# Performance work log

Hardware: AMD Instinct MI355X
Metric: run time of the kernel (lower is better)

The kernel has to match this reference:

```python
import jax, jax.numpy as jnp
import numpy as np

EMBED, HEADS, LEVELS, POINTS = 256, 8, 4, 4
HD = EMBED // HEADS
BS, NQ = 2, 16384
SHAPES = [(128, 128), (64, 64), (32, 32), (16, 16)]  # (H, W) per level
NV = sum(h * w for h, w in SHAPES)
EPS = 1e-5


def layernorm(x, g, b):
    mu = jnp.mean(x, -1, keepdims=True)
    var = jnp.mean((x - mu) ** 2, -1, keepdims=True)
    return (x - mu) / jnp.sqrt(var + EPS) * g + b


def bilinear_sample(vl, loc, H, W):
    # vl: (bs, heads, H*W, hd); loc: (bs, nq, heads, P, 2) normalized [0,1]
    # grid_sample semantics: align_corners=False, zero padding
    x = loc[..., 0] * W - 0.5
    y = loc[..., 1] * H - 0.5
    x0 = jnp.floor(x)
    y0 = jnp.floor(y)
    lx, ly = x - x0, y - y0
    x0 = x0.astype(jnp.int32)
    y0 = y0.astype(jnp.int32)
    gather = jax.vmap(jax.vmap(lambda t, i: t[i]))  # over (bs, heads)
    acc = None
    for dx, dy, w in ((0, 0, (1 - lx) * (1 - ly)), (1, 0, lx * (1 - ly)),
                      (0, 1, (1 - lx) * ly), (1, 1, lx * ly)):
        xi, yi = x0 + dx, y0 + dy
        valid = ((xi >= 0) & (xi < W) & (yi >= 0) & (yi < H)).astype(vl.dtype)
        idx = jnp.clip(yi, 0, H - 1) * W + jnp.clip(xi, 0, W - 1)
        idx = idx.transpose(0, 2, 1, 3)           # (bs, heads, nq, P)
        g = gather(vl, idx)                       # (bs, heads, nq, P, hd)
        wv = (w * valid).transpose(0, 2, 1, 3)[..., None]
        acc = g * wv if acc is None else acc + g * wv
    return acc


def forward(lidar_feat, feat_flatten, ref_2d, spatial_shapes, level_start_index,
            q_pose, W_off, b_off, W_attn, b_attn, W_val, b_val, W_out, b_out,
            ln1_g, ln1_b, ffn_w1, ffn_w2, ln2_g, ln2_b):
    identity = lidar_feat                         # (nq, bs, C)
    q = (lidar_feat + q_pose).transpose(1, 0, 2)  # (bs, nq, C)
    bs, nq, C = q.shape
    v = feat_flatten.transpose(1, 0, 2) @ W_val + b_val
    v = v.reshape(bs, -1, HEADS, HD)
    off = (q @ W_off + b_off).reshape(bs, nq, HEADS, LEVELS, POINTS, 2)
    aw = (q @ W_attn + b_attn).reshape(bs, nq, HEADS, LEVELS * POINTS)
    aw = jax.nn.softmax(aw, -1).reshape(bs, nq, HEADS, LEVELS, POINTS)
    ss = np.asarray(spatial_shapes)               # static level shapes
    lsi = np.asarray(level_start_index)
    norm = jnp.asarray(ss[:, ::-1].copy(), q.dtype)  # (L, 2) [W, H]
    loc = ref_2d[:, :, None, :, None, :] + off / norm[None, None, None, :, None, :]
    out = jnp.zeros((bs, nq, HEADS, HD), q.dtype)
    for l in range(LEVELS):
        H, W = int(ss[l, 0]), int(ss[l, 1])
        s = int(lsi[l])
        vl = v[:, s:s + H * W].transpose(0, 2, 1, 3)   # (bs, heads, HW, hd)
        sampled = bilinear_sample(vl, loc[:, :, :, l], H, W)
        out = out + jnp.einsum('bhqpd,bqhp->bqhd', sampled, aw[:, :, :, l, :])
    out = out.reshape(bs, nq, C) @ W_out + b_out
    out = out.transpose(1, 0, 2) + identity       # residual (dropout=eval noop)
    x = layernorm(out, ln1_g, ln1_b)
    x = layernorm(jnp.maximum(x @ ffn_w1, 0.0) @ ffn_w2 + x, ln2_g, ln2_b)
    return x


def setup_inputs():
    key = jax.random.key(0)
    ks = jax.random.split(key, 16)
    starts = np.cumsum([0] + [h * w for h, w in SHAPES])[:-1]
    d = {
        'lidar_feat': jax.random.normal(ks[0], (NQ, BS, EMBED), jnp.float32),
        'feat_flatten': jax.random.normal(ks[1], (NV, BS, EMBED), jnp.float32),
        'ref_2d': jax.random.uniform(ks[2], (BS, NQ, LEVELS, 2), jnp.float32),
        'spatial_shapes': jnp.array(SHAPES, jnp.int32),
        'level_start_index': jnp.array(starts, jnp.int32),
        'q_pose': jax.random.normal(ks[3], (NQ, BS, EMBED), jnp.float32),
        'W_off': 0.02 * jax.random.normal(ks[4], (EMBED, HEADS * LEVELS * POINTS * 2), jnp.float32),
        'b_off': 2.0 * jax.random.normal(ks[5], (HEADS * LEVELS * POINTS * 2,), jnp.float32),
        'W_attn': 0.02 * jax.random.normal(ks[6], (EMBED, HEADS * LEVELS * POINTS), jnp.float32),
        'b_attn': jnp.zeros((HEADS * LEVELS * POINTS,), jnp.float32),
        'W_val': 0.02 * jax.random.normal(ks[7], (EMBED, EMBED), jnp.float32),
        'b_val': jnp.zeros((EMBED,), jnp.float32),
        'W_out': 0.02 * jax.random.normal(ks[8], (EMBED, EMBED), jnp.float32),
        'b_out': jnp.zeros((EMBED,), jnp.float32),
        'ln1_g': jnp.ones((EMBED,), jnp.float32),
        'ln1_b': jnp.zeros((EMBED,), jnp.float32),
        'ffn_w1': 0.02 * jax.random.normal(ks[9], (EMBED, EMBED), jnp.float32),
        'ffn_w2': 0.02 * jax.random.normal(ks[10], (EMBED, EMBED), jnp.float32),
        'ln2_g': jnp.ones((EMBED,), jnp.float32),
        'ln2_b': jnp.zeros((EMBED,), jnp.float32),
    }
    return d


def reference(lidar_feat, feat_flatten, ref_2d, spatial_shapes, level_start_index,
              q_pose, W_off, b_off, W_attn, b_attn, W_val, b_val, W_out, b_out,
              ln1_g, ln1_b, ffn_w1, ffn_w2, ln2_g, ln2_b):
    return forward(lidar_feat, feat_flatten, ref_2d, spatial_shapes,
                   level_start_index, q_pose, W_off, b_off, W_attn, b_attn,
                   W_val, b_val, W_out, b_out, ln1_g, ln1_b, ffn_w1, ffn_w2,
                   ln2_g, ln2_b)
```

## Files before the change

kernel.cpp:

```cpp
#include <hip/hip_runtime.h>
#include <cstdint>

#define EMBED 256
#define HEADS 8
#define LEVELS 4
#define POINTS 4
#define BS 2
#define NQ 16384
#define NV 21760
#define MQ (BS*NQ)
#define MV (BS*NV)
#define VAL_BLK 340
#define OA_BLK  256

typedef __attribute__((ext_vector_type(8))) short short8;
typedef __attribute__((ext_vector_type(4))) float f32x4;

__device__ __forceinline__ unsigned short f2bf(float f) {
    unsigned int u = __float_as_uint(f);
    u = (u + 0x7FFFu + ((u >> 16) & 1u)) >> 16;
    return (unsigned short)u;
}
__device__ __forceinline__ float bf2f(unsigned short h) {
    return __uint_as_float(((unsigned int)h) << 16);
}
__device__ __forceinline__ void glds16(const unsigned short* g, unsigned short* l) {
    __builtin_amdgcn_global_load_lds((const __attribute__((address_space(1))) void*)g,
                                     (__attribute__((address_space(3))) void*)l, 16, 0, 0);
}

struct WtArgs {
    const float* src[6];
    unsigned short* dst[6];
    int n[6];
};
__global__ __launch_bounds__(256) void prep_wt(
    WtArgs a, const float* __restrict__ ref2d,
    int* __restrict__ bkt, int* __restrict__ hist)
{
    const int t = threadIdx.x, g = blockIdx.y, bx = blockIdx.x;
    if (g == 6) {
        if (bx < 64) {
#pragma unroll
            for (int i = 0; i < 2; ++i) {
                const int rb = bx * 512 + i * 256 + t;
                const float x = ref2d[(size_t)rb * 8 + 0];
                const float y = ref2d[(size_t)rb * 8 + 1];
                const int qx = min(15, max(0, (int)(x * 16.f)));
                const int qy = min(15, max(0, (int)(y * 16.f)));
                const int bv = (rb >> 14) * 256 + qy * 16 + qx;
                bkt[rb] = bv;
                atomicAdd(&hist[bv], 1);
            }
        }
        return;
    }
    const int N = a.n[g];
    const int e = bx * 256 + t;
    if (e >= 256 * N) return;
    const int k = e / N, n = e - k * N;
    a.dst[g][(size_t)n * 256 + k] = f2bf(a.src[g][e]);
}

template<int NCOLS>
__device__ __forceinline__ void gemm_core(
    unsigned short* As, unsigned short* Bs, int bx,
    const float* __restrict__ Af, const float* __restrict__ A2f, int inner,
    const unsigned short* __restrict__ Bt,
    const float* __restrict__ bias0, const float* __restrict__ bias1,
    float* __restrict__ outf, unsigned short* __restrict__ outh)
{
    constexpr int FN = NCOLS / 64;
    const int t = threadIdx.x, l = t & 63, w = t >> 6;
    const int wm = w >> 2, wn = w & 3;
    const int frow = l & 15, fgrp = l >> 4;
    const size_t brow = (size_t)bx * 128;

    const int fslot = fgrp ^ ((frow & 3) ^ ((frow >> 2) & 3));
    const int srow = l >> 2;
    const int sswz = (l & 3) ^ ((srow & 3) ^ ((srow >> 2) & 3));
    const unsigned short* gB0 = Bt + ((size_t)(w * 16 + srow)) * 256 + sswz * 8;

    const int arow_s = t >> 2, aslot_s = t & 3;
    const int grow = (int)brow + arow_s;
    const int bidx = grow / inner, nn = grow - bidx * inner;
    const float* srcA = Af + (size_t)(nn * BS + bidx) * 256;
    const float* srcA2 = A2f ? A2f + (size_t)(nn * BS + bidx) * 256 : nullptr;
    const int aswz_s = aslot_s ^ ((arow_s & 3) ^ ((arow_s >> 2) & 3));

    f32x4 acc[4][FN];
#pragma unroll
    for (int i = 0; i < 4; ++i)
#pragma unroll
        for (int j = 0; j < FN; ++j) acc[i][j] = f32x4{0.f, 0.f, 0.f, 0.f};

    float4 pA0 = *(const float4*)(srcA + aslot_s * 8);
    float4 pA1 = *(const float4*)(srcA + aslot_s * 8 + 4);
    float4 pC0, pC1;
    if (srcA2) { pC0 = *(const float4*)(srcA2 + aslot_s * 8);
                 pC1 = *(const float4*)(srcA2 + aslot_s * 8 + 4); }

    for (int k0 = 0; k0 < 256; k0 += 32) {
        glds16(gB0 + k0,         &Bs[w * 512]);
        glds16(gB0 + 32768 + k0, &Bs[(w + 8) * 512]);
        if constexpr (NCOLS == 384)
            glds16(gB0 + 65536 + k0, &Bs[(w + 16) * 512]);

        float c[8] = {pA0.x, pA0.y, pA0.z, pA0.w, pA1.x, pA1.y, pA1.z, pA1.w};
        if (srcA2) {
            c[0] += pC0.x; c[1] += pC0.y; c[2] += pC0.z; c[3] += pC0.w;
            c[4] += pC1.x; c[5] += pC1.y; c[6] += pC1.z; c[7] += pC1.w;
        }
        short8 pk;
#pragma unroll
        for (int i = 0; i < 8; ++i) pk[i] = (short)f2bf(c[i]);
        *reinterpret_cast<short8*>(&As[arow_s * 32 + aswz_s * 8]) = pk;
        if (k0 + 32 < 256) {
            pA0 = *(const float4*)(srcA + k0 + 32 + aslot_s * 8);
            pA1 = *(const float4*)(srcA + k0 + 32 + aslot_s * 8 + 4);
            if (srcA2) { pC0 = *(const float4*)(srcA2 + k0 + 32 + aslot_s * 8);
                         pC1 = *(const float4*)(srcA2 + k0 + 32 + aslot_s * 8 + 4); }
        }
        __syncthreads();

        short8 af[4]; short8 bq[FN];
#pragma unroll
        for (int fm = 0; fm < 4; ++fm)
            af[fm] = *reinterpret_cast<const short8*>(&As[(wm * 64 + fm * 16 + frow) * 32 + fslot * 8]);
#pragma unroll
        for (int fn = 0; fn < FN; ++fn)
            bq[fn] = *reinterpret_cast<const short8*>(&Bs[(wn * (NCOLS / 4) + fn * 16 + frow) * 32 + fslot * 8]);
#pragma unroll
        for (int fm = 0; fm < 4; ++fm)
#pragma unroll
            for (int fn = 0; fn < FN; ++fn)
                acc[fm][fn] = __builtin_amdgcn_mfma_f32_16x16x32_bf16(af[fm], bq[fn], acc[fm][fn], 0, 0, 0);
        __syncthreads();
    }

#pragma unroll
    for (int fn = 0; fn < FN; ++fn) {
        const int col = wn * (NCOLS / 4) + fn * 16 + frow;
        float b = 0.f;
        if (NCOLS == 384) b = (col < 256) ? bias0[col] : bias1[col - 256];
        else              b = bias0[col];
#pragma unroll
        for (int fm = 0; fm < 4; ++fm)
#pragma unroll
            for (int j = 0; j < 4; ++j) {
                const size_t row = brow + wm * 64 + fm * 16 + fgrp * 4 + j;
                const float x = acc[fm][fn][j] + b;
                if (outf) outf[row * NCOLS + col] = x;
                else      outh[row * NCOLS + col] = f2bf(x);
            }
    }
}

__global__ __launch_bounds__(512) void valoa_k(
    const float* __restrict__ feat, const float* __restrict__ lidar,
    const float* __restrict__ q_pose,
    const unsigned short* __restrict__ wt_val, const unsigned short* __restrict__ wt_oa,
    const float* __restrict__ b_val, const float* __restrict__ b_off,
    const float* __restrict__ b_attn,
    float* __restrict__ vb, unsigned short* __restrict__ oa,
    const int* __restrict__ hist, const int* __restrict__ bkt,
    int* __restrict__ perm)
{
    __shared__ unsigned short As[128 * 32];
    __shared__ unsigned short Bs[384 * 32];
    const int bx = blockIdx.x;
    if (bx < VAL_BLK) {
        gemm_core<256>(As, Bs, bx, feat, nullptr, NV, wt_val, b_val, nullptr, vb, nullptr);
    } else if (bx < VAL_BLK + OA_BLK) {
        gemm_core<384>(As, Bs, bx - VAL_BLK, lidar, q_pose, NQ, wt_oa, b_off, b_attn, nullptr, oa);
    } else {
        int* s   = (int*)As;
        int* cur = ((int*)As) + 512;
        const int t = threadIdx.x;
        const int v = hist[t];
        s[t] = v;
        __syncthreads();
        int acc = v;
#pragma unroll
        for (int o = 1; o < 512; o <<= 1) {
            const int add = (t >= o) ? s[t - o] : 0;
            __syncthreads();
            acc += add;
            s[t] = acc;
            __syncthreads();
        }
        cur[t] = acc - v;
        __syncthreads();
#pragma unroll 4
        for (int i = 0; i < 64; ++i) {
            const int rb = i * 512 + t;
            const int pos = atomicAdd(&cur[bkt[rb]], 1);
            perm[pos] = rb;
        }
    }
}

__global__ __launch_bounds__(256) void sampler_k(
    const unsigned short* __restrict__ oa,
    const float* __restrict__ ref2d,
    const float* __restrict__ v,
    const int* __restrict__ perm,
    unsigned short* __restrict__ outh)
{
    const int bid = blockIdx.x;
    const int sbid = (bid & 7) * (MQ / 4 / 8) + (bid >> 3);
    const int q0 = sbid * 4;
    const int t = threadIdx.x;

    __shared__ uint2 s_d[4][8][4][17];

#pragma unroll
    for (int it = 0; it < 2; ++it) {
        const int item = t + it * 256;
        const int tq = item >> 7, hlp = item & 127;
        const int h = hlp >> 4, lp = hlp & 15, li = lp >> 2;
        const int rb = perm[q0 + tq];
        const int b = rb >> 14;

        const float2 refv = *(const float2*)(ref2d + (size_t)rb * 8 + li * 2);
        const ushort2 offu = *(const ushort2*)(oa + (size_t)rb * 384 + hlp * 2);
        const float ax = bf2f(oa[(size_t)rb * 384 + 256 + hlp]);

        float m = ax;
#pragma unroll
        for (int o = 1; o < 16; o <<= 1) m = fmaxf(m, __shfl_xor(m, o));
        const float e = __expf(ax - m);
        float sden = e;
#pragma unroll
        for (int o = 1; o < 16; o <<= 1) sden += __shfl_xor(sden, o);
        const float a = e / sden;

        const int Wl[4]  = {128, 64, 32, 16};
        const int S0l[4] = {0, 16384, 20480, 21504};
        const int Wi = Wl[li]; const float Wf = (float)Wi;
        const float x = (refv.x + bf2f(offu.x) / Wf) * Wf - 0.5f;
        const float y = (refv.y + bf2f(offu.y) / Wf) * Wf - 0.5f;
        const float x0f = floorf(x), y0f = floorf(y);
        const float lx = x - x0f, ly = y - y0f;
        const int x0 = (int)x0f, y0 = (int)y0f;
        const float cw[4] = {(1.f - lx) * (1.f - ly) * a, lx * (1.f - ly) * a,
                             (1.f - lx) * ly * a,          lx * ly * a};
        const int base = b * NV + S0l[li];
#pragma unroll
        for (int c = 0; c < 4; ++c) {
            const int xi = x0 + (c & 1), yi = y0 + (c >> 1);
            const bool val = (xi >= 0) & (xi < Wi) & (yi >= 0) & (yi < Wi);
            const int xc = min(max(xi, 0), Wi - 1), yc = min(max(yi, 0), Wi - 1);
            const unsigned int ofs = (unsigned int)(base + yc * Wi + xc) * 1024u + h * 128u;
            s_d[tq][h][c][lp] = make_uint2(__float_as_uint(val ? cw[c] : 0.f), ofs);
        }
    }
    __syncthreads();

    const int tq = t >> 6, l = t & 63, h = l >> 3, dq = l & 7;
    const int rb = perm[q0 + tq], b = rb >> 14, qi = rb & (NQ - 1);
    const char* vq = (const char*)v + dq * 16u;
    float a0 = 0.f, a1 = 0.f, a2 = 0.f, a3 = 0.f;
#pragma unroll
    for (int c = 0; c < 4; ++c) {
#pragma unroll
        for (int i = 0; i < 16; ++i) {
            const uint2 dd = s_d[tq][h][c][i];
            const float4 raw = *(const float4*)(vq + dd.y);
            const float wgt = __uint_as_float(dd.x);
            a0 += wgt * raw.x;
            a1 += wgt * raw.y;
            a2 += wgt * raw.z;
            a3 += wgt * raw.w;
        }
    }
    ushort4 o; o.x = f2bf(a0); o.y = f2bf(a1); o.z = f2bf(a2); o.w = f2bf(a3);
    *(ushort4*)(outh + (size_t)(qi * BS + b) * 256 + h * 32 + dq * 4) = o;
}

__global__ __launch_bounds__(512) void mega_k(
    const unsigned short* __restrict__ smp, const float* __restrict__ lidar,
    const unsigned short* __restrict__ Wo, const unsigned short* __restrict__ W1,
    const unsigned short* __restrict__ W2, const float* __restrict__ b_out,
    const float* __restrict__ ln1g, const float* __restrict__ ln1b,
    const float* __restrict__ ln2g, const float* __restrict__ ln2b,
    float* __restrict__ outf)
{
    __shared__ unsigned short XH[64 * 256];
    __shared__ unsigned short Bs[256 * 32];
    __shared__ float2 sdLN[64][4];

    const int t = threadIdx.x, l = t & 63, w = t >> 6;
    const int wm = w >> 2, wn = w & 3;
    const int frow = l & 15, fgrp = l >> 4;
    const size_t brow = (size_t)blockIdx.x * 64;

    const int fslot = fgrp ^ ((frow & 3) ^ ((frow >> 2) & 3));
    const int srow = l >> 2;
    const int sswz = (l & 3) ^ ((srow & 3) ^ ((srow >> 2) & 3));

    const unsigned short* gA  = smp + (brow + (size_t)((w & 3) * 16 + srow)) * 256 + sswz * 8;
    const unsigned short* gWo = Wo + ((size_t)(w * 16 + srow)) * 256 + sswz * 8;
    const unsigned short* gW1 = W1 + ((size_t)(w * 16 + srow)) * 256 + sswz * 8;
    const unsigned short* gW2 = W2 + ((size_t)(w * 16 + srow)) * 256 + sswz * 8;

    f32x4 acc[2][4];
    f32x4 xres[2][4];

#pragma unroll
    for (int i = 0; i < 2; ++i)
#pragma unroll
        for (int j = 0; j < 4; ++j) acc[i][j] = f32x4{0.f, 0.f, 0.f, 0.f};

    for (int k0 = 0; k0 < 256; k0 += 32) {
        glds16(gWo + k0,         &Bs[w * 512]);
        glds16(gWo + 32768 + k0, &Bs[(w + 8) * 512]);
        if (w < 4) glds16(gA + k0, &XH[w * 512]);
        __syncthreads();
        short8 af[2], bq[4];
#pragma unroll
        for (int fm = 0; fm < 2; ++fm)
            af[fm] = *reinterpret_cast<const short8*>(&XH[(wm * 32 + fm * 16 + frow) * 32 + fslot * 8]);
#pragma unroll
        for (int fn = 0; fn < 4; ++fn)
            bq[fn] = *reinterpret_cast<const short8*>(&Bs[(wn * 64 + fn * 16 + frow) * 32 + fslot * 8]);
#pragma unroll
        for (int fm = 0; fm < 2; ++fm)
#pragma unroll
            for (int fn = 0; fn < 4; ++fn)
                acc[fm][fn] = __builtin_amdgcn_mfma_f32_16x16x32_bf16(af[fm], bq[fn], acc[fm][fn], 0, 0, 0);
        __syncthreads();
    }

#pragma unroll
    for (int fm = 0; fm < 2; ++fm)
#pragma unroll
        for (int fn = 0; fn < 4; ++fn) {
            const int col = wn * 64 + fn * 16 + frow;
            const float bv = b_out[col];
#pragma unroll
            for (int j = 0; j < 4; ++j) {
                const size_t row = brow + wm * 32 + fm * 16 + fgrp * 4 + j;
                acc[fm][fn][j] += bv + lidar[row * 256 + col];
            }
        }
#pragma unroll
    for (int fm = 0; fm < 2; ++fm)
#pragma unroll
        for (int j = 0; j < 4; ++j) {
            float s1 = 0.f, s2 = 0.f;
#pragma unroll
            for (int fn = 0; fn < 4; ++fn) { const float x = acc[fm][fn][j]; s1 += x; s2 += x * x; }
#pragma unroll
            for (int o = 1; o < 16; o <<= 1) { s1 += __shfl_xor(s1, o); s2 += __shfl_xor(s2, o); }
            if (frow == 0) sdLN[wm * 32 + fm * 16 + fgrp * 4 + j][wn] = make_float2(s1, s2);
        }
    __syncthreads();
#pragma unroll
    for (int fm = 0; fm < 2; ++fm)
#pragma unroll
        for (int j = 0; j < 4; ++j) {
            const int rl = wm * 32 + fm * 16 + fgrp * 4 + j;
            const float2 p0 = sdLN[rl][0], p1 = sdLN[rl][1], p2 = sdLN[rl][2], p3 = sdLN[rl][3];
            const float s1 = p0.x + p1.x + p2.x + p3.x;
            const float s2 = p0.y + p1.y + p2.y + p3.y;
            const float mu = s1 * (1.f / 256.f);
            const float var = s2 * (1.f / 256.f) - mu * mu;
            const float rstd = rsqrtf(var + 1e-5f);
#pragma unroll
            for (int fn = 0; fn < 4; ++fn) {
                const int col = wn * 64 + fn * 16 + frow;
                const float y = (acc[fm][fn][j] - mu) * rstd * ln1g[col] + ln1b[col];
                xres[fm][fn][j] = y;
                const int ss = (col >> 3) ^ (rl & 7);
                XH[rl * 256 + ss * 8 + (col & 7)] = f2bf(y);
            }
        }
    __syncthreads();

#pragma unroll
    for (int i = 0; i < 2; ++i)
#pragma unroll
        for (int j = 0; j < 4; ++j) acc[i][j] = f32x4{0.f, 0.f, 0.f, 0.f};

    for (int k0 = 0; k0 < 256; k0 += 32) {
        glds16(gW1 + k0,         &Bs[w * 512]);
        glds16(gW1 + 32768 + k0, &Bs[(w + 8) * 512]);
        __syncthreads();
        short8 af[2], bq[4];
#pragma unroll
        for (int fm = 0; fm < 2; ++fm) {
            const int row = wm * 32 + fm * 16 + frow;
            const int ss = ((k0 >> 3) + fgrp) ^ (row & 7);
            af[fm] = *reinterpret_cast<const short8*>(&XH[row * 256 + ss * 8]);
        }
#pragma unroll
        for (int fn = 0; fn < 4; ++fn)
            bq[fn] = *reinterpret_cast<const short8*>(&Bs[(wn * 64 + fn * 16 + frow) * 32 + fslot * 8]);
#pragma unroll
        for (int fm = 0; fm < 2; ++fm)
#pragma unroll
            for (int fn = 0; fn < 4; ++fn)
                acc[fm][fn] = __builtin_amdgcn_mfma_f32_16x16x32_bf16(af[fm], bq[fn], acc[fm][fn], 0, 0, 0);
        __syncthreads();
    }

#pragma unroll
    for (int fm = 0; fm < 2; ++fm)
#pragma unroll
        for (int fn = 0; fn < 4; ++fn) {
            const int col = wn * 64 + fn * 16 + frow;
#pragma unroll
            for (int j = 0; j < 4; ++j) {
                const int rl = wm * 32 + fm * 16 + fgrp * 4 + j;
                const int ss = (col >> 3) ^ (rl & 7);
                XH[rl * 256 + ss * 8 + (col & 7)] = f2bf(fmaxf(acc[fm][fn][j], 0.f));
            }
        }
    __syncthreads();

#pragma unroll
    for (int i = 0; i < 2; ++i)
#pragma unroll
        for (int j = 0; j < 4; ++j) acc[i][j] = f32x4{0.f, 0.f, 0.f, 0.f};

    for (int k0 = 0; k0 < 256; k0 += 32) {
        glds16(gW2 + k0,         &Bs[w * 512]);
        glds16(gW2 + 32768 + k0, &Bs[(w + 8) * 512]);
        __syncthreads();
        short8 af[2], bq[4];
#pragma unroll
        for (int fm = 0; fm < 2; ++fm) {
            const int row = wm * 32 + fm * 16 + frow;
            const int ss = ((k0 >> 3) + fgrp) ^ (row & 7);
            af[fm] = *reinterpret_cast<const short8*>(&XH[row * 256 + ss * 8]);
        }
#pragma unroll
        for (int fn = 0; fn < 4; ++fn)
            bq[fn] = *reinterpret_cast<const short8*>(&Bs[(wn * 64 + fn * 16 + frow) * 32 + fslot * 8]);
#pragma unroll
        for (int fm = 0; fm < 2; ++fm)
#pragma unroll
            for (int fn = 0; fn < 4; ++fn)
                acc[fm][fn] = __builtin_amdgcn_mfma_f32_16x16x32_bf16(af[fm], bq[fn], acc[fm][fn], 0, 0, 0);
        __syncthreads();
    }

#pragma unroll
    for (int fm = 0; fm < 2; ++fm)
#pragma unroll
        for (int fn = 0; fn < 4; ++fn)
#pragma unroll
            for (int j = 0; j < 4; ++j) acc[fm][fn][j] += xres[fm][fn][j];
#pragma unroll
    for (int fm = 0; fm < 2; ++fm)
#pragma unroll
        for (int j = 0; j < 4; ++j) {
            float s1 = 0.f, s2 = 0.f;
#pragma unroll
            for (int fn = 0; fn < 4; ++fn) { const float x = acc[fm][fn][j]; s1 += x; s2 += x * x; }
#pragma unroll
            for (int o = 1; o < 16; o <<= 1) { s1 += __shfl_xor(s1, o); s2 += __shfl_xor(s2, o); }
            if (frow == 0) sdLN[wm * 32 + fm * 16 + fgrp * 4 + j][wn] = make_float2(s1, s2);
        }
    __syncthreads();
#pragma unroll
    for (int fm = 0; fm < 2; ++fm)
#pragma unroll
        for (int j = 0; j < 4; ++j) {
            const int rl = wm * 32 + fm * 16 + fgrp * 4 + j;
            const float2 p0 = sdLN[rl][0], p1 = sdLN[rl][1], p2 = sdLN[rl][2], p3 = sdLN[rl][3];
            const float s1 = p0.x + p1.x + p2.x + p3.x;
            const float s2 = p0.y + p1.y + p2.y + p3.y;
            const float mu = s1 * (1.f / 256.f);
            const float var = s2 * (1.f / 256.f) - mu * mu;
            const float rstd = rsqrtf(var + 1e-5f);
            const size_t row = brow + rl;
#pragma unroll
            for (int fn = 0; fn < 4; ++fn) {
                const int col = wn * 64 + fn * 16 + frow;
                outf[row * 256 + col] = (acc[fm][fn][j] - mu) * rstd * ln2g[col] + ln2b[col];
            }
        }
}

extern "C" void kernel_launch(void* const* d_in, const int* in_sizes, int n_in,
                              void* d_out, int out_size, void* d_ws, size_t ws_size,
                              hipStream_t stream)
{
    const float* lidar  = (const float*)d_in[0];
    const float* feat   = (const float*)d_in[1];
    const float* ref2d  = (const float*)d_in[2];
    const float* q_pose = (const float*)d_in[5];
    const float* W_off  = (const float*)d_in[6];
    const float* b_off  = (const float*)d_in[7];
    const float* W_attn = (const float*)d_in[8];
    const float* b_attn = (const float*)d_in[9];
    const float* W_val  = (const float*)d_in[10];
    const float* b_val  = (const float*)d_in[11];
    const float* W_out  = (const float*)d_in[12];
    const float* b_out  = (const float*)d_in[13];
    const float* ln1_g  = (const float*)d_in[14];
    const float* ln1_b  = (const float*)d_in[15];
    const float* ffn_w1 = (const float*)d_in[16];
    const float* ffn_w2 = (const float*)d_in[17];
    const float* ln2_g  = (const float*)d_in[18];
    const float* ln2_b  = (const float*)d_in[19];

    float* out = (float*)d_out;
    char*  ws  = (char*)d_ws;

    float*          vb   = (float*)(ws + 0);
    unsigned short* oa   = (unsigned short*)(ws + 44564480);
    unsigned short* smp  = (unsigned short*)(ws + 69730304);
    unsigned short* wt   = (unsigned short*)(ws + 86507520);
    int* perm = (int*)(ws + 87228416);
    int* bkt  = (int*)(ws + 87359488);
    int* hist = (int*)(ws + 87490560);
    unsigned short* wt_val = wt;
    unsigned short* wt_oa  = wt + 65536;
    unsigned short* wt_out = wt + 163840;
    unsigned short* wt_f1  = wt + 229376;
    unsigned short* wt_f2  = wt + 294912;

    WtArgs wa;
    wa.src[0] = W_val;  wa.dst[0] = wt_val;          wa.n[0] = 256;
    wa.src[1] = W_off;  wa.dst[1] = wt_oa;           wa.n[1] = 256;
    wa.src[2] = W_attn; wa.dst[2] = wt_oa + 65536;   wa.n[2] = 128;
    wa.src[3] = W_out;  wa.dst[3] = wt_out;          wa.n[3] = 256;
    wa.src[4] = ffn_w1; wa.dst[4] = wt_f1;           wa.n[4] = 256;
    wa.src[5] = ffn_w2; wa.dst[5] = wt_f2;           wa.n[5] = 256;

    hipMemsetAsync(hist, 0, 2048, stream);

    prep_wt<<<dim3(384, 7), dim3(256), 0, stream>>>(wa, ref2d, bkt, hist);

    valoa_k<<<dim3(VAL_BLK + OA_BLK + 1), dim3(512), 0, stream>>>(
        feat, lidar, q_pose, wt_val, wt_oa, b_val, b_off, b_attn,
        vb, oa, hist, bkt, perm);

    sampler_k<<<dim3(MQ / 4), dim3(256), 0, stream>>>(oa, ref2d, vb, perm, smp);

    mega_k<<<dim3(MQ / 64), dim3(512), 0, stream>>>(
        smp, lidar, wt_out, wt_f1, wt_f2, b_out,
        ln1_g, ln1_b, ln2_g, ln2_b, out);
}
```

Baseline: 220.4 us.

## Store value projection and lidar residual in bf16 to halve sampler gather traffic

```diff
diff --git a/kernel.cpp b/kernel.cpp
--- a/kernel.cpp
+++ b/kernel.cpp
@@ -23,6 +23,12 @@
 }
 __device__ __forceinline__ float bf2f(unsigned short h) {
     return __uint_as_float(((unsigned int)h) << 16);
+}
+__device__ __forceinline__ float bflo(unsigned int u) {
+    return __uint_as_float(u << 16);
+}
+__device__ __forceinline__ float bfhi(unsigned int u) {
+    return __uint_as_float(u & 0xFFFF0000u);
 }
 __device__ __forceinline__ void glds16(const unsigned short* g, unsigned short* l) {
     __builtin_amdgcn_global_load_lds((const __attribute__((address_space(1))) void*)g,
@@ -68,7 +74,7 @@
     const float* __restrict__ Af, const float* __restrict__ A2f, int inner,
     const unsigned short* __restrict__ Bt,
     const float* __restrict__ bias0, const float* __restrict__ bias1,
-    float* __restrict__ outf, unsigned short* __restrict__ outh)
+    unsigned short* __restrict__ lidarb, unsigned short* __restrict__ outh)
 {
     constexpr int FN = NCOLS / 64;
     const int t = threadIdx.x, l = t & 63, w = t >> 6;
@@ -84,8 +90,9 @@
     const int arow_s = t >> 2, aslot_s = t & 3;
     const int grow = (int)brow + arow_s;
     const int bidx = grow / inner, nn = grow - bidx * inner;
-    const float* srcA = Af + (size_t)(nn * BS + bidx) * 256;
-    const float* srcA2 = A2f ? A2f + (size_t)(nn * BS + bidx) * 256 : nullptr;
+    const size_t srcrow = (size_t)(nn * BS + bidx) * 256;
+    const float* srcA = Af + srcrow;
+    const float* srcA2 = A2f ? A2f + srcrow : nullptr;
     const int aswz_s = aslot_s ^ ((arow_s & 3) ^ ((arow_s >> 2) & 3));
 
     f32x4 acc[4][FN];
@@ -105,6 +112,15 @@
         glds16(gB0 + 32768 + k0, &Bs[(w + 8) * 512]);
         if constexpr (NCOLS == 384)
             glds16(gB0 + 65536 + k0, &Bs[(w + 16) * 512]);
+
+        if (lidarb) {
+            short8 lk;
+            lk[0] = (short)f2bf(pA0.x); lk[1] = (short)f2bf(pA0.y);
+            lk[2] = (short)f2bf(pA0.z); lk[3] = (short)f2bf(pA0.w);
+            lk[4] = (short)f2bf(pA1.x); lk[5] = (short)f2bf(pA1.y);
+            lk[6] = (short)f2bf(pA1.z); lk[7] = (short)f2bf(pA1.w);
+            *reinterpret_cast<short8*>(lidarb + srcrow + k0 + aslot_s * 8) = lk;
+        }
 
         float c[8] = {pA0.x, pA0.y, pA0.z, pA0.w, pA1.x, pA1.y, pA1.z, pA1.w};
         if (srcA2) {
@@ -149,9 +165,7 @@
 #pragma unroll
             for (int j = 0; j < 4; ++j) {
                 const size_t row = brow + wm * 64 + fm * 16 + fgrp * 4 + j;
-                const float x = acc[fm][fn][j] + b;
-                if (outf) outf[row * NCOLS + col] = x;
-                else      outh[row * NCOLS + col] = f2bf(x);
+                outh[row * NCOLS + col] = f2bf(acc[fm][fn][j] + b);
             }
     }
 }
@@ -162,7 +176,8 @@
     const unsigned short* __restrict__ wt_val, const unsigned short* __restrict__ wt_oa,
     const float* __restrict__ b_val, const float* __restrict__ b_off,
     const float* __restrict__ b_attn,
-    float* __restrict__ vb, unsigned short* __restrict__ oa,
+    unsigned short* __restrict__ vb, unsigned short* __restrict__ oa,
+    unsigned short* __restrict__ lidarb,
     const int* __restrict__ hist, const int* __restrict__ bkt,
     int* __restrict__ perm)
 {
@@ -170,9 +185,9 @@
     __shared__ unsigned short Bs[384 * 32];
     const int bx = blockIdx.x;
     if (bx < VAL_BLK) {
-        gemm_core<256>(As, Bs, bx, feat, nullptr, NV, wt_val, b_val, nullptr, vb, nullptr);
+        gemm_core<256>(As, Bs, bx, feat, nullptr, NV, wt_val, b_val, nullptr, nullptr, vb);
     } else if (bx < VAL_BLK + OA_BLK) {
-        gemm_core<384>(As, Bs, bx - VAL_BLK, lidar, q_pose, NQ, wt_oa, b_off, b_attn, nullptr, oa);
+        gemm_core<384>(As, Bs, bx - VAL_BLK, lidar, q_pose, NQ, wt_oa, b_off, b_attn, lidarb, oa);
     } else {
         int* s   = (int*)As;
         int* cur = ((int*)As) + 512;
@@ -200,10 +215,10 @@
     }
 }
 
-__global__ __launch_bounds__(256) void sampler_k(
+__global__ __launch_bounds__(128) void sampler_k(
     const unsigned short* __restrict__ oa,
     const float* __restrict__ ref2d,
-    const float* __restrict__ v,
+    const unsigned short* __restrict__ v,
     const int* __restrict__ perm,
     unsigned short* __restrict__ outh)
 {
@@ -215,8 +230,8 @@
     __shared__ uint2 s_d[4][8][4][17];
 
 #pragma unroll
-    for (int it = 0; it < 2; ++it) {
-        const int item = t + it * 256;
+    for (int it = 0; it < 4; ++it) {
+        const int item = t + it * 128;
         const int tq = item >> 7, hlp = item & 127;
         const int h = hlp >> 4, lp = hlp & 15, li = lp >> 2;
         const int rb = perm[q0 + tq];
@@ -251,35 +266,40 @@
             const int xi = x0 + (c & 1), yi = y0 + (c >> 1);
             const bool val = (xi >= 0) & (xi < Wi) & (yi >= 0) & (yi < Wi);
             const int xc = min(max(xi, 0), Wi - 1), yc = min(max(yi, 0), Wi - 1);
-            const unsigned int ofs = (unsigned int)(base + yc * Wi + xc) * 1024u + h * 128u;
+            const unsigned int ofs = (unsigned int)(base + yc * Wi + xc) * 512u + h * 64u;
             s_d[tq][h][c][lp] = make_uint2(__float_as_uint(val ? cw[c] : 0.f), ofs);
         }
     }
     __syncthreads();
 
-    const int tq = t >> 6, l = t & 63, h = l >> 3, dq = l & 7;
+    const int tq = t >> 5, r = t & 31, h = r >> 2, dq = r & 3;
     const int rb = perm[q0 + tq], b = rb >> 14, qi = rb & (NQ - 1);
     const char* vq = (const char*)v + dq * 16u;
     float a0 = 0.f, a1 = 0.f, a2 = 0.f, a3 = 0.f;
+    float a4 = 0.f, a5 = 0.f, a6 = 0.f, a7 = 0.f;
 #pragma unroll
     for (int c = 0; c < 4; ++c) {
 #pragma unroll
         for (int i = 0; i < 16; ++i) {
             const uint2 dd = s_d[tq][h][c][i];
-            const float4 raw = *(const float4*)(vq + dd.y);
+            const uint4 raw = *(const uint4*)(vq + dd.y);
             const float wgt = __uint_as_float(dd.x);
-            a0 += wgt * raw.x;
-            a1 += wgt * raw.y;
-            a2 += wgt * raw.z;
-            a3 += wgt * raw.w;
-        }
-    }
-    ushort4 o; o.x = f2bf(a0); o.y = f2bf(a1); o.z = f2bf(a2); o.w = f2bf(a3);
-    *(ushort4*)(outh + (size_t)(qi * BS + b) * 256 + h * 32 + dq * 4) = o;
+            a0 += wgt * bflo(raw.x); a1 += wgt * bfhi(raw.x);
+            a2 += wgt * bflo(raw.y); a3 += wgt * bfhi(raw.y);
+            a4 += wgt * bflo(raw.z); a5 += wgt * bfhi(raw.z);
+            a6 += wgt * bflo(raw.w); a7 += wgt * bfhi(raw.w);
+        }
+    }
+    short8 o;
+    o[0] = (short)f2bf(a0); o[1] = (short)f2bf(a1);
+    o[2] = (short)f2bf(a2); o[3] = (short)f2bf(a3);
+    o[4] = (short)f2bf(a4); o[5] = (short)f2bf(a5);
+    o[6] = (short)f2bf(a6); o[7] = (short)f2bf(a7);
+    *reinterpret_cast<short8*>(outh + (size_t)(qi * BS + b) * 256 + h * 32 + dq * 8) = o;
 }
 
 __global__ __launch_bounds__(512) void mega_k(
-    const unsigned short* __restrict__ smp, const float* __restrict__ lidar,
+    const unsigned short* __restrict__ smp, const unsigned short* __restrict__ lidarb,
     const unsigned short* __restrict__ Wo, const unsigned short* __restrict__ W1,
     const unsigned short* __restrict__ W2, const float* __restrict__ b_out,
     const float* __restrict__ ln1g, const float* __restrict__ ln1b,
@@ -341,7 +361,7 @@
 #pragma unroll
             for (int j = 0; j < 4; ++j) {
                 const size_t row = brow + wm * 32 + fm * 16 + fgrp * 4 + j;
-                acc[fm][fn][j] += bv + lidar[row * 256 + col];
+                acc[fm][fn][j] += bv + bf2f(lidarb[row * 256 + col]);
             }
         }
 #pragma unroll
@@ -510,13 +530,14 @@
     float* out = (float*)d_out;
     char*  ws  = (char*)d_ws;
 
-    float*          vb   = (float*)(ws + 0);
-    unsigned short* oa   = (unsigned short*)(ws + 44564480);
-    unsigned short* smp  = (unsigned short*)(ws + 69730304);
-    unsigned short* wt   = (unsigned short*)(ws + 86507520);
-    int* perm = (int*)(ws + 87228416);
-    int* bkt  = (int*)(ws + 87359488);
-    int* hist = (int*)(ws + 87490560);
+    unsigned short* vb     = (unsigned short*)(ws + 0);
+    unsigned short* oa     = (unsigned short*)(ws + 22282240);
+    unsigned short* smp    = (unsigned short*)(ws + 47448064);
+    unsigned short* lidarb = (unsigned short*)(ws + 64225280);
+    unsigned short* wt     = (unsigned short*)(ws + 81002496);
+    int* perm = (int*)(ws + 81723392);
+    int* bkt  = (int*)(ws + 81854464);
+    int* hist = (int*)(ws + 81985536);
     unsigned short* wt_val = wt;
     unsigned short* wt_oa  = wt + 65536;
     unsigned short* wt_out = wt + 163840;
@@ -537,11 +558,11 @@
 
     valoa_k<<<dim3(VAL_BLK + OA_BLK + 1), dim3(512), 0, stream>>>(
         feat, lidar, q_pose, wt_val, wt_oa, b_val, b_off, b_attn,
-        vb, oa, hist, bkt, perm);
-
-    sampler_k<<<dim3(MQ / 4), dim3(256), 0, stream>>>(oa, ref2d, vb, perm, smp);
+        vb, oa, lidarb, hist, bkt, perm);
+
+    sampler_k<<<dim3(MQ / 4), dim3(128), 0, stream>>>(oa, ref2d, vb, perm, smp);
 
     mega_k<<<dim3(MQ / 64), dim3(512), 0, stream>>>(
-        smp, lidar, wt_out, wt_f1, wt_f2, b_out,
+        smp, lidarb, wt_out, wt_f1, wt_f2, b_out,
         ln1_g, ln1_b, ln2_g, ln2_b, out);
 }
```

New measurement: 216.6 us. Within noise of the previous version (-1.7%).
